# Performance work log

Hardware: AMD Instinct MI355X
Metric: run time of the kernel (lower is better)

The kernel has to match this reference:

```python
import jax, jax.numpy as jnp
import numpy as np

N_NODES = 100000


def gcn_layer(x, W, b, src, dst, n):
    # PyG GCNConv: h = x @ W, then D^{-1/2}(A+I)D^{-1/2} aggregation, then + b
    h = x @ W  # [N, out]
    ones = jnp.ones(src.shape[0], dtype=h.dtype)
    deg = jax.ops.segment_sum(ones, dst, num_segments=n) + 1.0  # +1 for self loop
    dinv = jax.lax.rsqrt(deg)  # [N]
    norm = dinv[src] * dinv[dst]  # [E]
    msgs = h[src] * norm[:, None]  # gather + scale, [E, out]
    agg = jax.ops.segment_sum(msgs, dst, num_segments=n)
    agg = agg + h * (dinv * dinv)[:, None]  # self-loop term
    return agg + b


def setup_inputs() -> dict:
    key = jax.random.key(0)
    k1, k2, k3, k4, k5, k6 = jax.random.split(key, 6)
    in_dim, h1, h2 = 256, 128, 64
    x = jax.random.normal(k1, (N_NODES, in_dim), dtype=jnp.float32)
    edge_index = jax.random.randint(k2, (2, 1600000), 0, N_NODES, dtype=jnp.int64)
    # Glorot-style init for weights, zeros for bias (PyG default)
    W1 = jax.random.normal(k3, (in_dim, h1), dtype=jnp.float32) / np.sqrt(in_dim)
    b1 = jnp.zeros((h1,), dtype=jnp.float32)
    W2 = jax.random.normal(k4, (h1, h2), dtype=jnp.float32) / np.sqrt(h1)
    b2 = jnp.zeros((h2,), dtype=jnp.float32)
    return {"x": x, "W1": W1, "b1": b1, "W2": W2, "b2": b2, "edge_index": edge_index}


def reference(x, W1, b1, W2, b2, edge_index):
    src, dst = edge_index[0], edge_index[1]
    n = x.shape[0]
    h = jax.nn.relu(gcn_layer(x, W1, b1, src, dst, n))
    h = jax.nn.relu(gcn_layer(h, W2, b2, src, dst, n))
    return h
```

## Files before the change

kernel.cpp:

```cpp
#include <hip/hip_runtime.h>
#include <hip/hip_bf16.h>


typedef __attribute__((ext_vector_type(8))) short bf16x8;
typedef __attribute__((ext_vector_type(4))) float f32x4;

__device__ inline unsigned short f2bf(float f) {
    unsigned u = __float_as_uint(f);
    u = (u + 0x7fff + ((u >> 16) & 1)) >> 16;
    return (unsigned short)u;
}
__device__ inline float bf2f(unsigned short h) {
    return __uint_as_float(((unsigned)h) << 16);
}
__device__ inline float bflo(unsigned u) { return __uint_as_float(u << 16); }
__device__ inline float bfhi(unsigned u) { return __uint_as_float(u & 0xffff0000u); }
__device__ inline unsigned pack_bf16_2(float lo, float hi) {
    return (unsigned)f2bf(lo) | ((unsigned)f2bf(hi) << 16);
}
__device__ inline void cvt8(const float* v, bf16x8& h8, bf16x8& l8) {
    #pragma unroll
    for (int j = 0; j < 8; ++j) {
        unsigned short h = f2bf(v[j]);
        h8[j] = (short)h;
        l8[j] = (short)f2bf(v[j] - bf2f(h));
    }
}

__global__ void prep_kernel(const int* __restrict__ dst, int* __restrict__ deg, int E,
        const float* __restrict__ W1, unsigned short* __restrict__ w1h,
        unsigned short* __restrict__ w1l,
        const float* __restrict__ W2, unsigned short* __restrict__ w2h,
        unsigned short* __restrict__ w2l) {
    const int W1B = (256 * 128) / 256;
    const int W2B = (128 * 64) / 256;
    int b = blockIdx.x;
    if (b < W1B) {
        int idx = b * 256 + threadIdx.x;
        int k = idx >> 7, n = idx & 127;
        float v = W1[idx];
        unsigned short h = f2bf(v);
        w1h[(size_t)n * 256 + k] = h;
        w1l[(size_t)n * 256 + k] = f2bf(v - bf2f(h));
    } else if (b < W1B + W2B) {
        int idx = (b - W1B) * 256 + threadIdx.x;
        int k = idx >> 6, n = idx & 63;
        float v = W2[idx];
        unsigned short h = f2bf(v);
        w2h[(size_t)n * 128 + k] = h;
        w2l[(size_t)n * 128 + k] = f2bf(v - bf2f(h));
    } else {
        int nb = gridDim.x - (W1B + W2B);
        int stride = nb * 256;
        for (int i = (b - W1B - W2B) * 256 + threadIdx.x; i < E; i += stride)
            atomicAdd(&deg[dst[i]], 1);
    }
}

__global__ __launch_bounds__(1024) void scan_partial_kernel(const int* __restrict__ deg,
        int* __restrict__ psum, float* __restrict__ dinv, int n) {
    __shared__ int wsum[16];
    int tid = threadIdx.x, wave = tid >> 6, lane = tid & 63;
    int i0 = blockIdx.x * 4096 + tid * 4;
    int v0 = 0, v1 = 0, v2 = 0, v3 = 0;
    if (i0 + 3 < n) {
        int4 v = *(const int4*)(deg + i0);
        v0 = v.x; v1 = v.y; v2 = v.z; v3 = v.w;
    } else {
        if (i0 + 0 < n) v0 = deg[i0 + 0];
        if (i0 + 1 < n) v1 = deg[i0 + 1];
        if (i0 + 2 < n) v2 = deg[i0 + 2];
        if (i0 + 3 < n) v3 = deg[i0 + 3];
    }
    if (i0 + 0 < n) dinv[i0 + 0] = 1.0f / sqrtf((float)v0 + 1.0f);
    if (i0 + 1 < n) dinv[i0 + 1] = 1.0f / sqrtf((float)v1 + 1.0f);
    if (i0 + 2 < n) dinv[i0 + 2] = 1.0f / sqrtf((float)v2 + 1.0f);
    if (i0 + 3 < n) dinv[i0 + 3] = 1.0f / sqrtf((float)v3 + 1.0f);
    int s = v0 + v1 + v2 + v3;
    #pragma unroll
    for (int off = 1; off < 64; off <<= 1) s += __shfl_xor(s, off, 64);
    if (lane == 0) wsum[wave] = s;
    __syncthreads();
    if (tid == 0) {
        int t = 0;
        #pragma unroll
        for (int w = 0; w < 16; ++w) t += wsum[w];
        psum[blockIdx.x] = t;
    }
}

__global__ void scan_base_kernel(int* __restrict__ psum, int* __restrict__ offs,
                                 int nb, int n) {
    int lane = threadIdx.x;
    int v = (lane < nb) ? psum[lane] : 0;
    int x = v;
    #pragma unroll
    for (int off = 1; off < 64; off <<= 1) {
        int y = __shfl_up(x, off, 64);
        if (lane >= off) x += y;
    }
    if (lane < nb) psum[lane] = x - v;
    if (lane == 63) offs[n] = x;
}

__global__ __launch_bounds__(1024) void scan_local_kernel(const int* __restrict__ deg,
        const int* __restrict__ psum, int* __restrict__ offs, int n) {
    __shared__ int wsum[16];
    int tid = threadIdx.x, wave = tid >> 6, lane = tid & 63;
    int i0 = blockIdx.x * 4096 + tid * 4;
    int v0 = 0, v1 = 0, v2 = 0, v3 = 0;
    if (i0 + 3 < n) {
        int4 v = *(const int4*)(deg + i0);
        v0 = v.x; v1 = v.y; v2 = v.z; v3 = v.w;
    } else {
        if (i0 + 0 < n) v0 = deg[i0 + 0];
        if (i0 + 1 < n) v1 = deg[i0 + 1];
        if (i0 + 2 < n) v2 = deg[i0 + 2];
        if (i0 + 3 < n) v3 = deg[i0 + 3];
    }
    int s = v0 + v1 + v2 + v3;
    int x = s;
    #pragma unroll
    for (int off = 1; off < 64; off <<= 1) {
        int y = __shfl_up(x, off, 64);
        if (lane >= off) x += y;
    }
    if (lane == 63) wsum[wave] = x;
    __syncthreads();
    int wbase = 0;
    #pragma unroll
    for (int w = 0; w < 16; ++w)
        if (w < wave) wbase += wsum[w];
    int ex = psum[blockIdx.x] + wbase + (x - s);
    if (i0 + 0 < n) offs[i0 + 0] = ex;
    if (i0 + 1 < n) offs[i0 + 1] = ex + v0;
    if (i0 + 2 < n) offs[i0 + 2] = ex + v0 + v1;
    if (i0 + 3 < n) offs[i0 + 3] = ex + v0 + v1 + v2;
}

__global__ __launch_bounds__(256) void fused_fill_gemm1(
        const int* __restrict__ src, const int* __restrict__ dst,
        const int* __restrict__ offs, int* __restrict__ cursor,
        int* __restrict__ csr, int E, int NF,
        const float* __restrict__ X,
        const unsigned short* __restrict__ Wh, const unsigned short* __restrict__ Wl,
        const float* __restrict__ dinv, unsigned short* __restrict__ G, int M) {
    if ((int)blockIdx.x < NF) {
        int stride = NF * 256;
        for (int i = blockIdx.x * 256 + threadIdx.x; i < E; i += stride) {
            int d = dst[i];
            int pos = offs[d] + atomicAdd(&cursor[d], 1);
            csr[pos] = src[i];
        }
        return;
    }
    constexpr int K = 256;
    const int bid = blockIdx.x - NF;
    const int tid = threadIdx.x;
    const int wv = tid >> 6, ln = tid & 63;
    const int l16 = ln & 15, kseg = ln >> 4;
    const int r0 = bid * 128 + wv * 32;

    int rA0 = r0 + l16;       if (rA0 >= M) rA0 = M - 1;
    int rA1 = r0 + 16 + l16;  if (rA1 >= M) rA1 = M - 1;
    const float* pA0 = X + (size_t)rA0 * K + kseg * 8;
    const float* pA1 = X + (size_t)rA1 * K + kseg * 8;

    f32x4 acc[2][8];
    #pragma unroll
    for (int a = 0; a < 2; ++a)
        #pragma unroll
        for (int b = 0; b < 8; ++b) acc[a][b] = 0;

    #pragma unroll 2
    for (int k0 = 0; k0 < K; k0 += 32) {
        bf16x8 ah[2], al[2];
        {
            float4 qa = *(const float4*)(pA0 + k0);
            float4 qb = *(const float4*)(pA0 + k0 + 4);
            float v[8] = {qa.x, qa.y, qa.z, qa.w, qb.x, qb.y, qb.z, qb.w};
            cvt8(v, ah[0], al[0]);
        }
        {
            float4 qa = *(const float4*)(pA1 + k0);
            float4 qb = *(const float4*)(pA1 + k0 + 4);
            float v[8] = {qa.x, qa.y, qa.z, qa.w, qb.x, qb.y, qb.z, qb.w};
            cvt8(v, ah[1], al[1]);
        }
        #pragma unroll
        for (int tc = 0; tc < 8; ++tc) {
            size_t wo = (size_t)(tc * 16 + l16) * K + k0 + kseg * 8;
            bf16x8 bh = *(const bf16x8*)(Wh + wo);
            bf16x8 bl = *(const bf16x8*)(Wl + wo);
            #pragma unroll
            for (int tr = 0; tr < 2; ++tr) {
                acc[tr][tc] = __builtin_amdgcn_mfma_f32_16x16x32_bf16(ah[tr], bh, acc[tr][tc], 0, 0, 0);
                acc[tr][tc] = __builtin_amdgcn_mfma_f32_16x16x32_bf16(al[tr], bh, acc[tr][tc], 0, 0, 0);
                acc[tr][tc] = __builtin_amdgcn_mfma_f32_16x16x32_bf16(ah[tr], bl, acc[tr][tc], 0, 0, 0);
            }
        }
    }

    #pragma unroll
    for (int tr = 0; tr < 2; ++tr) {
        int rbase = r0 + tr * 16 + (ln >> 4) * 4;
        #pragma unroll
        for (int r = 0; r < 4; ++r) {
            int row = rbase + r;
            if (row < M) {
                float dv = dinv[row];
                #pragma unroll
                for (int tc = 0; tc < 8; ++tc)
                    G[(size_t)row * 128 + tc * 16 + l16] = f2bf(acc[tr][tc][r] * dv);
            }
        }
    }
}

__global__ __launch_bounds__(256) void gemm2_kernel(const unsigned short* __restrict__ H,
        const unsigned short* __restrict__ Wh, const unsigned short* __restrict__ Wl,
        const float* __restrict__ dinv, unsigned short* __restrict__ G, int M) {
    constexpr int K = 128;
    const int tid = threadIdx.x;
    const int wv = tid >> 6, ln = tid & 63;
    const int l16 = ln & 15, kseg = ln >> 4;
    const int r0 = blockIdx.x * 128 + wv * 32;

    int rA0 = r0 + l16;       if (rA0 >= M) rA0 = M - 1;
    int rA1 = r0 + 16 + l16;  if (rA1 >= M) rA1 = M - 1;
    const unsigned short* pA0 = H + (size_t)rA0 * K + kseg * 8;
    const unsigned short* pA1 = H + (size_t)rA1 * K + kseg * 8;

    f32x4 acc[2][4];
    #pragma unroll
    for (int a = 0; a < 2; ++a)
        #pragma unroll
        for (int b = 0; b < 4; ++b) acc[a][b] = 0;

    #pragma unroll
    for (int k0 = 0; k0 < K; k0 += 32) {
        bf16x8 a0 = *(const bf16x8*)(pA0 + k0);
        bf16x8 a1 = *(const bf16x8*)(pA1 + k0);
        #pragma unroll
        for (int tc = 0; tc < 4; ++tc) {
            size_t wo = (size_t)(tc * 16 + l16) * K + k0 + kseg * 8;
            bf16x8 bh = *(const bf16x8*)(Wh + wo);
            bf16x8 bl = *(const bf16x8*)(Wl + wo);
            acc[0][tc] = __builtin_amdgcn_mfma_f32_16x16x32_bf16(a0, bh, acc[0][tc], 0, 0, 0);
            acc[0][tc] = __builtin_amdgcn_mfma_f32_16x16x32_bf16(a0, bl, acc[0][tc], 0, 0, 0);
            acc[1][tc] = __builtin_amdgcn_mfma_f32_16x16x32_bf16(a1, bh, acc[1][tc], 0, 0, 0);
            acc[1][tc] = __builtin_amdgcn_mfma_f32_16x16x32_bf16(a1, bl, acc[1][tc], 0, 0, 0);
        }
    }

    #pragma unroll
    for (int tr = 0; tr < 2; ++tr) {
        int rbase = r0 + tr * 16 + (ln >> 4) * 4;
        #pragma unroll
        for (int r = 0; r < 4; ++r) {
            int row = rbase + r;
            if (row < M) {
                float dv = dinv[row];
                #pragma unroll
                for (int tc = 0; tc < 4; ++tc)
                    G[(size_t)row * 64 + tc * 16 + l16] = f2bf(acc[tr][tc][r] * dv);
            }
        }
    }
}

__global__ __launch_bounds__(256) void aggregate128_kernel(const unsigned* __restrict__ G,
        const int* __restrict__ csr, const int* __restrict__ offs,
        const float* __restrict__ dinv, const float* __restrict__ bias,
        unsigned* __restrict__ out, int n) {
    int wave = threadIdx.x >> 6, lane = threadIdx.x & 63;
    int node = blockIdx.x * 4 + wave;
    if (node >= n) return;
    int beg = offs[node], end = offs[node + 1];

    unsigned u = G[(size_t)node * 64 + lane];
    float a0 = bflo(u), a1 = bfhi(u);
    int e = beg;
    for (; e + 4 <= end; e += 4) {
        int s0 = csr[e], s1 = csr[e + 1], s2 = csr[e + 2], s3 = csr[e + 3];
        unsigned u0 = G[(size_t)s0 * 64 + lane];
        unsigned u1 = G[(size_t)s1 * 64 + lane];
        unsigned u2 = G[(size_t)s2 * 64 + lane];
        unsigned u3 = G[(size_t)s3 * 64 + lane];
        a0 += (bflo(u0) + bflo(u1)) + (bflo(u2) + bflo(u3));
        a1 += (bfhi(u0) + bfhi(u1)) + (bfhi(u2) + bfhi(u3));
    }
    for (; e < end; ++e) {
        unsigned u0 = G[(size_t)csr[e] * 64 + lane];
        a0 += bflo(u0);
        a1 += bfhi(u0);
    }
    float di = dinv[node];
    float rx = fmaxf(fmaf(a0, di, bias[lane * 2 + 0]), 0.0f);
    float ry = fmaxf(fmaf(a1, di, bias[lane * 2 + 1]), 0.0f);
    out[(size_t)node * 64 + lane] = pack_bf16_2(rx, ry);
}

__global__ __launch_bounds__(256) void aggregate64_kernel(const unsigned* __restrict__ G,
        const int* __restrict__ csr, const int* __restrict__ offs,
        const float* __restrict__ dinv, const float* __restrict__ bias,
        float* __restrict__ out, int n) {
    int wave = threadIdx.x >> 6, lane = threadIdx.x & 63;
    int node = blockIdx.x * 4 + wave;
    if (node >= n) return;
    int beg = offs[node], end = offs[node + 1];
    int half = lane >> 5, col = lane & 31;

    float a0 = 0.0f, a1 = 0.0f;
    if (half == 0) {
        unsigned u = G[(size_t)node * 32 + col];
        a0 = bflo(u); a1 = bfhi(u);
    }
    int e = beg;
    for (; e + 4 <= end; e += 4) {
        int sA = csr[e + half], sB = csr[e + 2 + half];
        unsigned uA = G[(size_t)sA * 32 + col];
        unsigned uB = G[(size_t)sB * 32 + col];
        a0 += bflo(uA) + bflo(uB);
        a1 += bfhi(uA) + bfhi(uB);
    }
    if (e + 2 <= end) {
        int sA = csr[e + half];
        unsigned uA = G[(size_t)sA * 32 + col];
        a0 += bflo(uA);
        a1 += bfhi(uA);
        e += 2;
    }
    if (e < end && half == 0) {
        unsigned uA = G[(size_t)csr[e] * 32 + col];
        a0 += bflo(uA);
        a1 += bfhi(uA);
    }
    a0 += __shfl_down(a0, 32, 64);
    a1 += __shfl_down(a1, 32, 64);
    if (half == 0) {
        float di = dinv[node];
        float2 r;
        r.x = fmaxf(fmaf(a0, di, bias[col * 2 + 0]), 0.0f);
        r.y = fmaxf(fmaf(a1, di, bias[col * 2 + 1]), 0.0f);
        ((float2*)(out + (size_t)node * 64))[col] = r;
    }
}

extern "C" void kernel_launch(void* const* d_in, const int* in_sizes, int n_in,
                              void* d_out, int out_size, void* d_ws, size_t ws_size,
                              hipStream_t stream) {
    const float* x  = (const float*)d_in[0];
    const float* W1 = (const float*)d_in[1];
    const float* b1 = (const float*)d_in[2];
    const float* W2 = (const float*)d_in[3];
    const float* b2 = (const float*)d_in[4];
    const int* edge = (const int*)d_in[5];

    const int IN = 256, H1 = 128, H2 = 64;
    const int E = in_sizes[5] / 2;
    const int N = in_sizes[0] / IN;
    const int* srcp = edge;
    const int* dstp = edge + E;

    char* ws = (char*)d_ws;
    auto alignup = [](size_t v) { return (v + 255) & ~(size_t)255; };
    size_t off = 0;
    size_t degSz = alignup((size_t)N * 4);
    int*            deg    = (int*)(ws + off);            off += degSz;
    int*            cursor = (int*)(ws + off);            off += degSz;
    int*            offs   = (int*)(ws + off);            off += alignup(((size_t)N + 1) * 4);
    float*          dinv   = (float*)(ws + off);          off += degSz;
    int*            psum   = (int*)(ws + off);            off += alignup(64 * 4);
    int*            csr    = (int*)(ws + off);            off += alignup((size_t)E * 4);
    unsigned short* wt1h   = (unsigned short*)(ws + off); off += alignup((size_t)IN * H1 * 2);
    unsigned short* wt1l   = (unsigned short*)(ws + off); off += alignup((size_t)IN * H1 * 2);
    unsigned short* wt2h   = (unsigned short*)(ws + off); off += alignup((size_t)H1 * H2 * 2);
    unsigned short* wt2l   = (unsigned short*)(ws + off); off += alignup((size_t)H1 * H2 * 2);
    unsigned short* g1     = (unsigned short*)(ws + off); off += alignup((size_t)N * H1 * 2);
    unsigned*       h1b    = (unsigned*)(ws + off);       off += alignup((size_t)N * (H1 / 2) * 4);
    unsigned short* g2     = g1;

    hipMemsetAsync(deg, 0, 2 * degSz, stream);

    int hgrid = 2048;
    int sb = (N + 4095) / 4096;

    prep_kernel<<<160 + hgrid, 256, 0, stream>>>(dstp, deg, E, W1, wt1h, wt1l,
                                                 W2, wt2h, wt2l);
    scan_partial_kernel<<<sb, 1024, 0, stream>>>(deg, psum, dinv, N);
    scan_base_kernel<<<1, 64, 0, stream>>>(psum, offs, sb, N);
    scan_local_kernel<<<sb, 1024, 0, stream>>>(deg, psum, offs, N);

    const int NF = 1024;
    const int NG = (N + 127) / 128;
    fused_fill_gemm1<<<NF + NG, 256, 0, stream>>>(srcp, dstp, offs, cursor, csr, E,
                                                  NF, x, wt1h, wt1l, dinv, g1, N);

    int agrid = (N + 3) / 4;
    aggregate128_kernel<<<agrid, 256, 0, stream>>>((const unsigned*)g1, csr, offs,
                                                   dinv, b1, h1b, N);
    gemm2_kernel<<<NG, 256, 0, stream>>>((const unsigned short*)h1b, wt2h, wt2l,
                                         dinv, g2, N);
    aggregate64_kernel<<<agrid, 256, 0, stream>>>((const unsigned*)g2, csr, offs,
                                                  dinv, b2, (float*)d_out, N);
}
```

Measured before the change: 526.1 us.

## Fold scan base into local scan and interleave fill/GEMM blocks

Removes the single-wave scan_base kernel launch: each scan_local block now sums the per-block partials itself to get its base offset, and block 0 writes the total. The fused CSR-fill and GEMM1 kernel now alternates fill and GEMM blocks by blockIdx parity, with as many fill blocks as GEMM blocks (NG instead of 1024). This is meant to cut one launch and to overlap memory-bound atomic scatter with the compute-bound GEMM on each CU. The redundant partial-sum loop per block is tiny (sb≈25).

```diff
diff --git a/kernel.cpp b/kernel.cpp
--- a/kernel.cpp
+++ b/kernel.cpp
@@ -89,25 +89,20 @@
     }
 }
 
-__global__ void scan_base_kernel(int* __restrict__ psum, int* __restrict__ offs,
-                                 int nb, int n) {
-    int lane = threadIdx.x;
-    int v = (lane < nb) ? psum[lane] : 0;
-    int x = v;
-    #pragma unroll
-    for (int off = 1; off < 64; off <<= 1) {
-        int y = __shfl_up(x, off, 64);
-        if (lane >= off) x += y;
-    }
-    if (lane < nb) psum[lane] = x - v;
-    if (lane == 63) offs[n] = x;
-}
-
 __global__ __launch_bounds__(1024) void scan_local_kernel(const int* __restrict__ deg,
-        const int* __restrict__ psum, int* __restrict__ offs, int n) {
+        const int* __restrict__ psum, int* __restrict__ offs, int n, int sb) {
     __shared__ int wsum[16];
     int tid = threadIdx.x, wave = tid >> 6, lane = tid & 63;
-    int i0 = blockIdx.x * 4096 + tid * 4;
+    int bid = blockIdx.x;
+    int base = 0, total = 0;
+    for (int w = 0; w < sb; ++w) {
+        int t = psum[w];
+        if (w < bid) base += t;
+        total += t;
+    }
+    if (bid == 0 && tid == 0) offs[n] = total;
+
+    int i0 = bid * 4096 + tid * 4;
     int v0 = 0, v1 = 0, v2 = 0, v3 = 0;
     if (i0 + 3 < n) {
         int4 v = *(const int4*)(deg + i0);
@@ -131,7 +126,7 @@
     #pragma unroll
     for (int w = 0; w < 16; ++w)
         if (w < wave) wbase += wsum[w];
-    int ex = psum[blockIdx.x] + wbase + (x - s);
+    int ex = base + wbase + (x - s);
     if (i0 + 0 < n) offs[i0 + 0] = ex;
     if (i0 + 1 < n) offs[i0 + 1] = ex + v0;
     if (i0 + 2 < n) offs[i0 + 2] = ex + v0 + v1;
@@ -141,13 +136,14 @@
 __global__ __launch_bounds__(256) void fused_fill_gemm1(
         const int* __restrict__ src, const int* __restrict__ dst,
         const int* __restrict__ offs, int* __restrict__ cursor,
-        int* __restrict__ csr, int E, int NF,
+        int* __restrict__ csr, int E, int NG,
         const float* __restrict__ X,
         const unsigned short* __restrict__ Wh, const unsigned short* __restrict__ Wl,
         const float* __restrict__ dinv, unsigned short* __restrict__ G, int M) {
-    if ((int)blockIdx.x < NF) {
-        int stride = NF * 256;
-        for (int i = blockIdx.x * 256 + threadIdx.x; i < E; i += stride) {
+    const int bid2 = blockIdx.x >> 1;
+    if (!(blockIdx.x & 1)) {
+        int stride = NG * 256;
+        for (int i = bid2 * 256 + threadIdx.x; i < E; i += stride) {
             int d = dst[i];
             int pos = offs[d] + atomicAdd(&cursor[d], 1);
             csr[pos] = src[i];
@@ -155,11 +151,10 @@
         return;
     }
     constexpr int K = 256;
-    const int bid = blockIdx.x - NF;
     const int tid = threadIdx.x;
     const int wv = tid >> 6, ln = tid & 63;
     const int l16 = ln & 15, kseg = ln >> 4;
-    const int r0 = bid * 128 + wv * 32;
+    const int r0 = bid2 * 128 + wv * 32;
 
     int rA0 = r0 + l16;       if (rA0 >= M) rA0 = M - 1;
     int rA1 = r0 + 16 + l16;  if (rA1 >= M) rA1 = M - 1;
@@ -389,13 +384,11 @@
     prep_kernel<<<160 + hgrid, 256, 0, stream>>>(dstp, deg, E, W1, wt1h, wt1l,
                                                  W2, wt2h, wt2l);
     scan_partial_kernel<<<sb, 1024, 0, stream>>>(deg, psum, dinv, N);
-    scan_base_kernel<<<1, 64, 0, stream>>>(psum, offs, sb, N);
-    scan_local_kernel<<<sb, 1024, 0, stream>>>(deg, psum, offs, N);
-
-    const int NF = 1024;
+    scan_local_kernel<<<sb, 1024, 0, stream>>>(deg, psum, offs, N, sb);
+
     const int NG = (N + 127) / 128;
-    fused_fill_gemm1<<<NF + NG, 256, 0, stream>>>(srcp, dstp, offs, cursor, csr, E,
-                                                  NF, x, wt1h, wt1l, dinv, g1, N);
+    fused_fill_gemm1<<<2 * NG, 256, 0, stream>>>(srcp, dstp, offs, cursor, csr, E,
+                                                 NG, x, wt1h, wt1l, dinv, g1, N);
 
     int agrid = (N + 3) / 4;
     aggregate128_kernel<<<agrid, 256, 0, stream>>>((const unsigned*)g1, csr, offs,
```

New measurement: 544.0 us. +3.4%, slower.
